# Kernel tuning notes

Hardware: AMD Instinct MI355X
Metric: run time of the kernel (lower is better)

## Reference

```python
import jax, jax.numpy as jnp
import numpy as np

N = 100000
D = 128
E = 1600000
NUM_STEPS = 8
LAM0 = 1.0
LAM1 = 1.0
ALPHA = 1.0 / (1.0 + 0.0 + LAM0 + LAM1)  # args.alp == 0 path


def setup_inputs() -> dict:
    key = jax.random.key(0)
    ks = jax.random.split(key, 12)
    X = jax.random.normal(ks[0], (N, D), dtype=jnp.float32)
    # H init: normal(0, 1/in_features) + I  (notresidual=False branch)
    H1 = jax.random.normal(ks[1], (D, D), dtype=jnp.float32) * (1.0 / D) + jnp.eye(D, dtype=jnp.float32)
    H2 = jax.random.normal(ks[2], (D, D), dtype=jnp.float32) * (1.0 / D) + jnp.eye(D, dtype=jnp.float32)
    w_beta = jax.random.uniform(ks[3], (E,), dtype=jnp.float32)
    w_gamma = jax.random.uniform(ks[4], (E,), dtype=jnp.float32)
    d_beta = jax.random.uniform(ks[5], (N,), dtype=jnp.float32)
    d_gamma = jax.random.uniform(ks[6], (N,), dtype=jnp.float32)
    src_beta = jax.random.randint(ks[7], (E,), 0, N, dtype=jnp.int32)
    dst_beta = jax.random.randint(ks[8], (E,), 0, N, dtype=jnp.int32)
    src_gamma = jax.random.randint(ks[9], (E,), 0, N, dtype=jnp.int32)
    dst_gamma = jax.random.randint(ks[10], (E,), 0, N, dtype=jnp.int32)
    return {"X": X, "H1": H1, "H2": H2, "w_beta": w_beta, "w_gamma": w_gamma,
            "d_beta": d_beta, "d_gamma": d_gamma,
            "src_beta": src_beta, "dst_beta": dst_beta,
            "src_gamma": src_gamma, "dst_gamma": dst_gamma}


def _spmm(w, src, dst, Y):
    # (sparse A) @ Y with A[dst, src] = w
    return jax.ops.segment_sum(w[:, None] * Y[src], dst, num_segments=N)


def reference(X, H1, H2, w_beta, w_gamma, d_beta, d_gamma,
              src_beta, dst_beta, src_gamma, dst_gamma):
    # Q_tild = lam0*D_beta + lam1*D_gamma + I  (diagonal)
    q = LAM0 * d_beta + LAM1 * d_gamma + 1.0  # [N]
    S1 = H1 + H1.T
    P1 = H1 @ H1.T
    S2 = H2 + H2.T
    P2 = H2 @ H2.T
    Y0 = X
    Y = X
    for _ in range(NUM_STEPS):
        AbY = _spmm(w_beta, src_beta, dst_beta, Y)    # A_beta @ Y
        AgY = _spmm(w_gamma, src_gamma, dst_gamma, Y)  # A_gamma @ Y
        term_beta = AbY @ S1 - d_beta[:, None] * (Y @ P1)
        # L_gamma @ Y = D_gamma@Y - A_gamma@Y
        term_gamma = (d_gamma[:, None] * Y - AgY
                      + AgY @ S2 - d_gamma[:, None] * (Y @ P2))
        Y_hat = LAM0 * term_beta + Y0 + LAM1 * term_gamma
        Y = (1.0 - ALPHA) * Y + ALPHA * (Y_hat / q[:, None])
    return Y
```

## Files before the change

kernel.cpp:

```cpp
#include <hip/hip_runtime.h>
#include <cstdint>
#include <cstddef>

#define DD 128


__global__ void count2_k(const int* __restrict__ dstb, const int* __restrict__ dstg,
                         int* __restrict__ degb, int* __restrict__ degg, int E, int gE) {
    int b = blockIdx.x;
    const int* dst = (b < gE) ? dstb : dstg;
    int* deg = (b < gE) ? degb : degg;
    int i = ((b < gE) ? b : b - gE) * blockDim.x + threadIdx.x;
    if (i < E) atomicAdd(&deg[dst[i]], 1);
}

__global__ __launch_bounds__(1024) void scan2_k(const int* __restrict__ degb,
                                                const int* __restrict__ degg,
                                                int* __restrict__ rpb, int* __restrict__ rpg,
                                                int* __restrict__ curb, int* __restrict__ curg,
                                                int n) {
    const int* deg = (blockIdx.x == 0) ? degb : degg;
    int* rp = (blockIdx.x == 0) ? rpb : rpg;
    int* cur = (blockIdx.x == 0) ? curb : curg;
    __shared__ int sums[1024];
    int tid = threadIdx.x;
    int per = (n + 1023) >> 10;
    int start = tid * per;
    int end = min(start + per, n);
    int s = 0;
    for (int i = start; i < end; ++i) s += deg[i];
    sums[tid] = s;
    __syncthreads();
    for (int off = 1; off < 1024; off <<= 1) {
        int v = (tid >= off) ? sums[tid - off] : 0;
        __syncthreads();
        sums[tid] += v;
        __syncthreads();
    }
    int pre = (tid == 0) ? 0 : sums[tid - 1];
    for (int i = start; i < end; ++i) {
        rp[i] = pre;
        cur[i] = pre;
        pre += deg[i];
    }
    if (end == n) rp[n] = pre;
}

__global__ void fill2_k(const int* __restrict__ srcb, const int* __restrict__ dstb,
                        const float* __restrict__ wb,
                        const int* __restrict__ srcg, const int* __restrict__ dstg,
                        const float* __restrict__ wg,
                        int* __restrict__ curb, int* __restrict__ curg,
                        int2* __restrict__ eb, int2* __restrict__ eg, int E, int gE) {
    int b = blockIdx.x;
    bool isb = (b < gE);
    const int* src = isb ? srcb : srcg;
    const int* dst = isb ? dstb : dstg;
    const float* w = isb ? wb : wg;
    int* cur = isb ? curb : curg;
    int2* edges = isb ? eb : eg;
    int i = (isb ? b : b - gE) * blockDim.x + threadIdx.x;
    if (i < E) {
        int d = dst[i];
        int pos = atomicAdd(&cur[d], 1);
        edges[pos] = make_int2(src[i], __float_as_int(w[i]));
    }
}


__global__ __launch_bounds__(256) void prep_k(const float* __restrict__ H,
                                              float* __restrict__ P,
                                              float* __restrict__ S) {
    int idx = blockIdx.x * 256 + threadIdx.x;
    int i = idx >> 7, j = idx & 127;
    float acc = 0.f;
    for (int k = 0; k < DD; ++k) acc += H[i * DD + k] * H[j * DD + k];
    P[idx] = acc;
    S[idx] = H[i * DD + j] + H[j * DD + i];
}


__global__ __launch_bounds__(256) void spmm_k(const int* __restrict__ rp,
                                              const int2* __restrict__ edges,
                                              const float* __restrict__ Y,
                                              float* __restrict__ out, int n) {
    int node = blockIdx.x * 4 + (threadIdx.x >> 6);
    if (node >= n) return;
    int lane = threadIdx.x & 63;
    int beg = rp[node], end = rp[node + 1];
    float a0 = 0.f, a1 = 0.f;
    int j = beg;
    for (; j + 8 <= end; j += 8) {
        int2 e0 = edges[j + 0], e1 = edges[j + 1], e2 = edges[j + 2], e3 = edges[j + 3];
        int2 e4 = edges[j + 4], e5 = edges[j + 5], e6 = edges[j + 6], e7 = edges[j + 7];
        float2 f0 = *((const float2*)(Y + (size_t)e0.x * DD) + lane);
        float2 f1 = *((const float2*)(Y + (size_t)e1.x * DD) + lane);
        float2 f2 = *((const float2*)(Y + (size_t)e2.x * DD) + lane);
        float2 f3 = *((const float2*)(Y + (size_t)e3.x * DD) + lane);
        float2 f4 = *((const float2*)(Y + (size_t)e4.x * DD) + lane);
        float2 f5 = *((const float2*)(Y + (size_t)e5.x * DD) + lane);
        float2 f6 = *((const float2*)(Y + (size_t)e6.x * DD) + lane);
        float2 f7 = *((const float2*)(Y + (size_t)e7.x * DD) + lane);
        float w0 = __int_as_float(e0.y), w1 = __int_as_float(e1.y);
        float w2 = __int_as_float(e2.y), w3 = __int_as_float(e3.y);
        float w4 = __int_as_float(e4.y), w5 = __int_as_float(e5.y);
        float w6 = __int_as_float(e6.y), w7 = __int_as_float(e7.y);
        a0 += w0 * f0.x; a1 += w0 * f0.y;
        a0 += w1 * f1.x; a1 += w1 * f1.y;
        a0 += w2 * f2.x; a1 += w2 * f2.y;
        a0 += w3 * f3.x; a1 += w3 * f3.y;
        a0 += w4 * f4.x; a1 += w4 * f4.y;
        a0 += w5 * f5.x; a1 += w5 * f5.y;
        a0 += w6 * f6.x; a1 += w6 * f6.y;
        a0 += w7 * f7.x; a1 += w7 * f7.y;
    }
    for (; j + 4 <= end; j += 4) {
        int2 e0 = edges[j + 0], e1 = edges[j + 1], e2 = edges[j + 2], e3 = edges[j + 3];
        float2 f0 = *((const float2*)(Y + (size_t)e0.x * DD) + lane);
        float2 f1 = *((const float2*)(Y + (size_t)e1.x * DD) + lane);
        float2 f2 = *((const float2*)(Y + (size_t)e2.x * DD) + lane);
        float2 f3 = *((const float2*)(Y + (size_t)e3.x * DD) + lane);
        float w0 = __int_as_float(e0.y), w1 = __int_as_float(e1.y);
        float w2 = __int_as_float(e2.y), w3 = __int_as_float(e3.y);
        a0 += w0 * f0.x; a1 += w0 * f0.y;
        a0 += w1 * f1.x; a1 += w1 * f1.y;
        a0 += w2 * f2.x; a1 += w2 * f2.y;
        a0 += w3 * f3.x; a1 += w3 * f3.y;
    }
    for (; j < end; ++j) {
        int2 e = edges[j];
        float2 f = *((const float2*)(Y + (size_t)e.x * DD) + lane);
        float wv = __int_as_float(e.y);
        a0 += wv * f.x; a1 += wv * f.y;
    }
    *((float2*)(out + (size_t)node * DD) + lane) = make_float2(a0, a1);
}


#define ATS 68
#define BS 160

__global__ __launch_bounds__(128, 2) void dense_k(
    const float* __restrict__ Y, const float* __restrict__ X,
    const float* __restrict__ Ab, const float* __restrict__ Ag,
    const float* __restrict__ db, const float* __restrict__ dg,
    const float* __restrict__ P1, const float* __restrict__ P2,
    const float* __restrict__ S1, const float* __restrict__ S2,
    float* __restrict__ Yn, int n)
{
    __shared__ float At[32 * ATS];
    __shared__ float B1[32 * BS];
    __shared__ float B2[32 * BS];

    const int tid = threadIdx.x;
    const int cg = tid & 15;
    const int rg = tid >> 4;
    const int row0 = blockIdx.x * 64;

    float aP1[8][8], aP2[8][8], aS[8][8];
#pragma unroll
    for (int i = 0; i < 8; ++i)
#pragma unroll
        for (int j = 0; j < 8; ++j) { aP1[i][j] = 0.f; aP2[i][j] = 0.f; aS[i][j] = 0.f; }

    auto stageA = [&](const float* __restrict__ G, int kq) {
        int r = tid >> 1;
        int kh = (tid & 1) * 16;
        int rowc = min(row0 + r, n - 1);
        const float* gp = G + (size_t)rowc * DD + kq * 32 + kh;
#pragma unroll
        for (int u = 0; u < 4; ++u) {
            float4 v = *reinterpret_cast<const float4*>(gp + 4 * u);
            int kb = kh + 4 * u;
            At[(kb + 0) * ATS + r] = v.x;
            At[(kb + 1) * ATS + r] = v.y;
            At[(kb + 2) * ATS + r] = v.z;
            At[(kb + 3) * ATS + r] = v.w;
        }
    };
    auto stageB = [&](const float* __restrict__ M, float* __restrict__ Bd, int kq) {
        int kl = tid >> 2;
        int cb = (tid & 3) * 32;
        const float* gp = M + (size_t)(kq * 32 + kl) * DD + cb;
        float* bp = Bd + kl * BS;
#pragma unroll
        for (int u = 0; u < 8; ++u) {
            float4 v = *reinterpret_cast<const float4*>(gp + 4 * u);
            int c = cb + 4 * u;
            float vv[4] = {v.x, v.y, v.z, v.w};
#pragma unroll
            for (int q = 0; q < 4; ++q) {
                int cc = c + q;
                bp[10 * (cc >> 3) + (cc & 7)] = vv[q];
            }
        }
    };

    const int abase = rg * 8;
    const int bbase = 10 * cg;

    for (int kq = 0; kq < 4; ++kq) {
        if (kq) __syncthreads();
        stageA(Y, kq);
        stageB(P1, B1, kq);
        stageB(P2, B2, kq);
        __syncthreads();
#pragma unroll 2
        for (int kl = 0; kl < 32; ++kl) {
            float a[8], b1[8], b2[8];
            *reinterpret_cast<float4*>(&a[0]) = *reinterpret_cast<const float4*>(&At[kl * ATS + abase]);
            *reinterpret_cast<float4*>(&a[4]) = *reinterpret_cast<const float4*>(&At[kl * ATS + abase + 4]);
#pragma unroll
            for (int m = 0; m < 4; ++m) {
                *reinterpret_cast<float2*>(&b1[2 * m]) = *reinterpret_cast<const float2*>(&B1[kl * BS + bbase + 2 * m]);
                *reinterpret_cast<float2*>(&b2[2 * m]) = *reinterpret_cast<const float2*>(&B2[kl * BS + bbase + 2 * m]);
            }
#pragma unroll
            for (int i = 0; i < 8; ++i)
#pragma unroll
                for (int j = 0; j < 8; ++j) {
                    aP1[i][j] += a[i] * b1[j];
                    aP2[i][j] += a[i] * b2[j];
                }
        }
    }
    __syncthreads();

    for (int kq = 0; kq < 4; ++kq) {
        if (kq) __syncthreads();
        stageA(Ab, kq);
        stageB(S1, B1, kq);
        __syncthreads();
#pragma unroll 2
        for (int kl = 0; kl < 32; ++kl) {
            float a[8], b1[8];
            *reinterpret_cast<float4*>(&a[0]) = *reinterpret_cast<const float4*>(&At[kl * ATS + abase]);
            *reinterpret_cast<float4*>(&a[4]) = *reinterpret_cast<const float4*>(&At[kl * ATS + abase + 4]);
#pragma unroll
            for (int m = 0; m < 4; ++m)
                *reinterpret_cast<float2*>(&b1[2 * m]) = *reinterpret_cast<const float2*>(&B1[kl * BS + bbase + 2 * m]);
#pragma unroll
            for (int i = 0; i < 8; ++i)
#pragma unroll
                for (int j = 0; j < 8; ++j) aS[i][j] += a[i] * b1[j];
        }
    }
    __syncthreads();

    for (int kq = 0; kq < 4; ++kq) {
        if (kq) __syncthreads();
        stageA(Ag, kq);
        stageB(S2, B1, kq);
        __syncthreads();
#pragma unroll 2
        for (int kl = 0; kl < 32; ++kl) {
            float a[8], b1[8];
            *reinterpret_cast<float4*>(&a[0]) = *reinterpret_cast<const float4*>(&At[kl * ATS + abase]);
            *reinterpret_cast<float4*>(&a[4]) = *reinterpret_cast<const float4*>(&At[kl * ATS + abase + 4]);
#pragma unroll
            for (int m = 0; m < 4; ++m)
                *reinterpret_cast<float2*>(&b1[2 * m]) = *reinterpret_cast<const float2*>(&B1[kl * BS + bbase + 2 * m]);
#pragma unroll
            for (int i = 0; i < 8; ++i)
#pragma unroll
                for (int j = 0; j < 8; ++j) aS[i][j] += a[i] * b1[j];
        }
    }

    const float AL = 1.0f / 3.0f;
#pragma unroll
    for (int i = 0; i < 8; ++i) {
        int row = row0 + rg * 8 + i;
        if (row < n) {
            float dbv = db[row], dgv = dg[row];
            float aq = AL / (dbv + dgv + 1.0f);
            size_t off = (size_t)row * DD + cg * 8;
            float4 y0 = *reinterpret_cast<const float4*>(Y + off);
            float4 y1 = *reinterpret_cast<const float4*>(Y + off + 4);
            float4 x0 = *reinterpret_cast<const float4*>(X + off);
            float4 x1 = *reinterpret_cast<const float4*>(X + off + 4);
            float4 g0 = *reinterpret_cast<const float4*>(Ag + off);
            float4 g1 = *reinterpret_cast<const float4*>(Ag + off + 4);
            float yv[8] = {y0.x, y0.y, y0.z, y0.w, y1.x, y1.y, y1.z, y1.w};
            float xv[8] = {x0.x, x0.y, x0.z, x0.w, x1.x, x1.y, x1.z, x1.w};
            float gv[8] = {g0.x, g0.y, g0.z, g0.w, g1.x, g1.y, g1.z, g1.w};
            float ov[8];
#pragma unroll
            for (int j = 0; j < 8; ++j) {
                float yhat = aS[i][j] - dbv * aP1[i][j] - dgv * aP2[i][j]
                             + xv[j] + dgv * yv[j] - gv[j];
                ov[j] = (1.0f - AL) * yv[j] + yhat * aq;
            }
            *reinterpret_cast<float4*>(Yn + off) = make_float4(ov[0], ov[1], ov[2], ov[3]);
            *reinterpret_cast<float4*>(Yn + off + 4) = make_float4(ov[4], ov[5], ov[6], ov[7]);
        }
    }
}


extern "C" void kernel_launch(void* const* d_in, const int* in_sizes, int n_in,
                              void* d_out, int out_size, void* d_ws, size_t ws_size,
                              hipStream_t stream) {
    const float* X   = (const float*)d_in[0];
    const float* H1  = (const float*)d_in[1];
    const float* H2  = (const float*)d_in[2];
    const float* wb  = (const float*)d_in[3];
    const float* wg  = (const float*)d_in[4];
    const float* db  = (const float*)d_in[5];
    const float* dg  = (const float*)d_in[6];
    const int* srcb  = (const int*)d_in[7];
    const int* dstb  = (const int*)d_in[8];
    const int* srcg  = (const int*)d_in[9];
    const int* dstg  = (const int*)d_in[10];
    const int N = in_sizes[5];
    const int E = in_sizes[3];
    float* Yout = (float*)d_out;

    char* p = (char*)d_ws;
    auto alloc = [&](size_t b) -> void* {
        void* r = (void*)p;
        p += (b + 255) & ~(size_t)255;
        return r;
    };
    float* P1 = (float*)alloc((size_t)DD * DD * 4);
    float* S1 = (float*)alloc((size_t)DD * DD * 4);
    float* P2 = (float*)alloc((size_t)DD * DD * 4);
    float* S2 = (float*)alloc((size_t)DD * DD * 4);
    int* degb = (int*)alloc((size_t)N * 4);
    int* degg = (int*)alloc((size_t)N * 4);
    int* rpb  = (int*)alloc((size_t)(N + 1) * 4);
    int* rpg  = (int*)alloc((size_t)(N + 1) * 4);
    int* curb = (int*)alloc((size_t)N * 4);
    int* curg = (int*)alloc((size_t)N * 4);
    int2* eb  = (int2*)alloc((size_t)E * 8);
    int2* eg  = (int2*)alloc((size_t)E * 8);
    float* AbY = (float*)alloc((size_t)N * DD * 4);
    float* AgY = (float*)alloc((size_t)N * DD * 4);
    float* Yw  = (float*)alloc((size_t)N * DD * 4);

    hipMemsetAsync(degb, 0, (size_t)N * 4, stream);
    hipMemsetAsync(degg, 0, (size_t)N * 4, stream);

    int gE = (E + 255) / 256;
    count2_k<<<2 * gE, 256, 0, stream>>>(dstb, dstg, degb, degg, E, gE);
    scan2_k<<<2, 1024, 0, stream>>>(degb, degg, rpb, rpg, curb, curg, N);
    fill2_k<<<2 * gE, 256, 0, stream>>>(srcb, dstb, wb, srcg, dstg, wg,
                                        curb, curg, eb, eg, E, gE);
    prep_k<<<64, 256, 0, stream>>>(H1, P1, S1);
    prep_k<<<64, 256, 0, stream>>>(H2, P2, S2);

    const float* Ycur = X;
    float* Ybufs[2] = {Yw, Yout};
    int gs = (N + 3) / 4;
    int gd = (N + 63) / 64;
    for (int s = 0; s < 8; ++s) {
        spmm_k<<<gs, 256, 0, stream>>>(rpb, eb, Ycur, AbY, N);
        spmm_k<<<gs, 256, 0, stream>>>(rpg, eg, Ycur, AgY, N);
        float* Yn = Ybufs[s & 1];
        dense_k<<<gd, 128, 0, stream>>>(Ycur, X, AbY, AgY, db, dg,
                                        P1, P2, S1, S2, Yn, N);
        Ycur = Yn;
    }
}
```

Before: 4.297 ms.

## Fuse SpMM gathers into dense step kernel, keeping aggregated tiles in shared memory

Merges the two SpMM kernels and the dense update into one per-step kernel. Each 256-thread block gathers A_beta@Y and A_gamma@Y rows for its 64-node tile straight into shared memory and multiplies by S1/S2 there, and the -A_gamma@Y term is read from shared memory. This removes the N x 128 AbY/AgY intermediates and their global write and read, plus two launches per step. The tradeoff is that the gather is serialized inside the block with syncs between phases. Occupancy now depends on the 256-thread block and its larger shared footprint (about 48 KB) instead of separate gather kernels with many small blocks, so load-latency hiding during the gather may be weaker.

```diff
diff --git a/kernel.cpp b/kernel.cpp
--- a/kernel.cpp
+++ b/kernel.cpp
@@ -3,6 +3,9 @@
 #include <cstddef>
 
 #define DD 128
+#define ATS 68
+#define ARS 132
+#define BQS 132
 
 
 __global__ void count2_k(const int* __restrict__ dstb, const int* __restrict__ dstg,
@@ -80,219 +83,173 @@
 }
 
 
-__global__ __launch_bounds__(256) void spmm_k(const int* __restrict__ rp,
-                                              const int2* __restrict__ edges,
-                                              const float* __restrict__ Y,
-                                              float* __restrict__ out, int n) {
-    int node = blockIdx.x * 4 + (threadIdx.x >> 6);
-    if (node >= n) return;
-    int lane = threadIdx.x & 63;
-    int beg = rp[node], end = rp[node + 1];
-    float a0 = 0.f, a1 = 0.f;
-    int j = beg;
-    for (; j + 8 <= end; j += 8) {
-        int2 e0 = edges[j + 0], e1 = edges[j + 1], e2 = edges[j + 2], e3 = edges[j + 3];
-        int2 e4 = edges[j + 4], e5 = edges[j + 5], e6 = edges[j + 6], e7 = edges[j + 7];
-        float2 f0 = *((const float2*)(Y + (size_t)e0.x * DD) + lane);
-        float2 f1 = *((const float2*)(Y + (size_t)e1.x * DD) + lane);
-        float2 f2 = *((const float2*)(Y + (size_t)e2.x * DD) + lane);
-        float2 f3 = *((const float2*)(Y + (size_t)e3.x * DD) + lane);
-        float2 f4 = *((const float2*)(Y + (size_t)e4.x * DD) + lane);
-        float2 f5 = *((const float2*)(Y + (size_t)e5.x * DD) + lane);
-        float2 f6 = *((const float2*)(Y + (size_t)e6.x * DD) + lane);
-        float2 f7 = *((const float2*)(Y + (size_t)e7.x * DD) + lane);
-        float w0 = __int_as_float(e0.y), w1 = __int_as_float(e1.y);
-        float w2 = __int_as_float(e2.y), w3 = __int_as_float(e3.y);
-        float w4 = __int_as_float(e4.y), w5 = __int_as_float(e5.y);
-        float w6 = __int_as_float(e6.y), w7 = __int_as_float(e7.y);
-        a0 += w0 * f0.x; a1 += w0 * f0.y;
-        a0 += w1 * f1.x; a1 += w1 * f1.y;
-        a0 += w2 * f2.x; a1 += w2 * f2.y;
-        a0 += w3 * f3.x; a1 += w3 * f3.y;
-        a0 += w4 * f4.x; a1 += w4 * f4.y;
-        a0 += w5 * f5.x; a1 += w5 * f5.y;
-        a0 += w6 * f6.x; a1 += w6 * f6.y;
-        a0 += w7 * f7.x; a1 += w7 * f7.y;
-    }
-    for (; j + 4 <= end; j += 4) {
-        int2 e0 = edges[j + 0], e1 = edges[j + 1], e2 = edges[j + 2], e3 = edges[j + 3];
-        float2 f0 = *((const float2*)(Y + (size_t)e0.x * DD) + lane);
-        float2 f1 = *((const float2*)(Y + (size_t)e1.x * DD) + lane);
-        float2 f2 = *((const float2*)(Y + (size_t)e2.x * DD) + lane);
-        float2 f3 = *((const float2*)(Y + (size_t)e3.x * DD) + lane);
-        float w0 = __int_as_float(e0.y), w1 = __int_as_float(e1.y);
-        float w2 = __int_as_float(e2.y), w3 = __int_as_float(e3.y);
-        a0 += w0 * f0.x; a1 += w0 * f0.y;
-        a0 += w1 * f1.x; a1 += w1 * f1.y;
-        a0 += w2 * f2.x; a1 += w2 * f2.y;
-        a0 += w3 * f3.x; a1 += w3 * f3.y;
-    }
-    for (; j < end; ++j) {
-        int2 e = edges[j];
-        float2 f = *((const float2*)(Y + (size_t)e.x * DD) + lane);
-        float wv = __int_as_float(e.y);
-        a0 += wv * f.x; a1 += wv * f.y;
-    }
-    *((float2*)(out + (size_t)node * DD) + lane) = make_float2(a0, a1);
-}
-
-
-#define ATS 68
-#define BS 160
-
-__global__ __launch_bounds__(128, 2) void dense_k(
-    const float* __restrict__ Y, const float* __restrict__ X,
-    const float* __restrict__ Ab, const float* __restrict__ Ag,
+__global__ __launch_bounds__(256, 3) void step_k(
+    const float* __restrict__ Yc, const float* __restrict__ X,
+    const int* __restrict__ rpb, const int2* __restrict__ eb,
+    const int* __restrict__ rpg, const int2* __restrict__ eg,
     const float* __restrict__ db, const float* __restrict__ dg,
     const float* __restrict__ P1, const float* __restrict__ P2,
     const float* __restrict__ S1, const float* __restrict__ S2,
     float* __restrict__ Yn, int n)
 {
-    __shared__ float At[32 * ATS];
-    __shared__ float B1[32 * BS];
-    __shared__ float B2[32 * BS];
+    __shared__ float At[DD * ATS];
+    __shared__ float U[32 * ARS];
 
     const int tid = threadIdx.x;
+    const int lane = tid & 63;
+    const int wv = tid >> 6;
     const int cg = tid & 15;
     const int rg = tid >> 4;
     const int row0 = blockIdx.x * 64;
 
-    float aP1[8][8], aP2[8][8], aS[8][8];
-#pragma unroll
-    for (int i = 0; i < 8; ++i)
-#pragma unroll
-        for (int j = 0; j < 8; ++j) { aP1[i][j] = 0.f; aP2[i][j] = 0.f; aS[i][j] = 0.f; }
-
-    auto stageA = [&](const float* __restrict__ G, int kq) {
-        int r = tid >> 1;
-        int kh = (tid & 1) * 16;
+    float aS[4][8], aP1[4][8], aP2[4][8];
+#pragma unroll
+    for (int i = 0; i < 4; ++i)
+#pragma unroll
+        for (int j = 0; j < 8; ++j) { aS[i][j] = 0.f; aP1[i][j] = 0.f; aP2[i][j] = 0.f; }
+
+    auto gatherA = [&](const int* __restrict__ rp, const int2* __restrict__ edges) {
+        for (int h = 0; h < 2; ++h) {
+#pragma unroll 1
+            for (int it = 0; it < 8; ++it) {
+                int r = wv * 8 + it;
+                int node = row0 + h * 32 + r;
+                float a0 = 0.f, a1 = 0.f;
+                if (node < n) {
+                    int beg = rp[node], end = rp[node + 1];
+                    int j = beg;
+                    for (; j + 4 <= end; j += 4) {
+                        int2 e0 = edges[j + 0], e1 = edges[j + 1];
+                        int2 e2 = edges[j + 2], e3 = edges[j + 3];
+                        float2 f0 = *((const float2*)(Yc + (size_t)e0.x * DD) + lane);
+                        float2 f1 = *((const float2*)(Yc + (size_t)e1.x * DD) + lane);
+                        float2 f2 = *((const float2*)(Yc + (size_t)e2.x * DD) + lane);
+                        float2 f3 = *((const float2*)(Yc + (size_t)e3.x * DD) + lane);
+                        float w0 = __int_as_float(e0.y), w1 = __int_as_float(e1.y);
+                        float w2 = __int_as_float(e2.y), w3 = __int_as_float(e3.y);
+                        a0 += w0 * f0.x; a1 += w0 * f0.y;
+                        a0 += w1 * f1.x; a1 += w1 * f1.y;
+                        a0 += w2 * f2.x; a1 += w2 * f2.y;
+                        a0 += w3 * f3.x; a1 += w3 * f3.y;
+                    }
+                    for (; j < end; ++j) {
+                        int2 e = edges[j];
+                        float2 f = *((const float2*)(Yc + (size_t)e.x * DD) + lane);
+                        float wv2 = __int_as_float(e.y);
+                        a0 += wv2 * f.x; a1 += wv2 * f.y;
+                    }
+                }
+                *reinterpret_cast<float2*>(&U[r * ARS + 2 * lane]) = make_float2(a0, a1);
+            }
+            __syncthreads();
+            {
+                int r = tid & 31;
+                int cb = (tid >> 5) * 16;
+#pragma unroll
+                for (int u = 0; u < 4; ++u) {
+                    float4 v = *reinterpret_cast<const float4*>(&U[r * ARS + cb + 4 * u]);
+                    int c = cb + 4 * u;
+                    At[(c + 0) * ATS + h * 32 + r] = v.x;
+                    At[(c + 1) * ATS + h * 32 + r] = v.y;
+                    At[(c + 2) * ATS + h * 32 + r] = v.z;
+                    At[(c + 3) * ATS + h * 32 + r] = v.w;
+                }
+            }
+            __syncthreads();
+        }
+    };
+
+    auto stageY = [&]() {
+        int r = tid >> 2;
         int rowc = min(row0 + r, n - 1);
-        const float* gp = G + (size_t)rowc * DD + kq * 32 + kh;
-#pragma unroll
-        for (int u = 0; u < 4; ++u) {
-            float4 v = *reinterpret_cast<const float4*>(gp + 4 * u);
-            int kb = kh + 4 * u;
-            At[(kb + 0) * ATS + r] = v.x;
-            At[(kb + 1) * ATS + r] = v.y;
-            At[(kb + 2) * ATS + r] = v.z;
-            At[(kb + 3) * ATS + r] = v.w;
+        const float* gp = Yc + (size_t)rowc * DD;
+#pragma unroll
+        for (int i = 0; i < 8; ++i) {
+            int c = ((tid & 3) << 2) + (i << 4);
+            float4 v = *reinterpret_cast<const float4*>(gp + c);
+            At[(c + 0) * ATS + r] = v.x;
+            At[(c + 1) * ATS + r] = v.y;
+            At[(c + 2) * ATS + r] = v.z;
+            At[(c + 3) * ATS + r] = v.w;
         }
     };
-    auto stageB = [&](const float* __restrict__ M, float* __restrict__ Bd, int kq) {
-        int kl = tid >> 2;
-        int cb = (tid & 3) * 32;
-        const float* gp = M + (size_t)(kq * 32 + kl) * DD + cb;
-        float* bp = Bd + kl * BS;
-#pragma unroll
-        for (int u = 0; u < 8; ++u) {
-            float4 v = *reinterpret_cast<const float4*>(gp + 4 * u);
-            int c = cb + 4 * u;
-            float vv[4] = {v.x, v.y, v.z, v.w};
-#pragma unroll
-            for (int q = 0; q < 4; ++q) {
-                int cc = c + q;
-                bp[10 * (cc >> 3) + (cc & 7)] = vv[q];
-            }
+
+    auto gemm = [&](const float* __restrict__ M, float (&acc)[4][8]) {
+#pragma unroll 1
+        for (int kq = 0; kq < 4; ++kq) {
+            {
+                int kl = tid & 31;
+                int cb = (tid >> 5) * 16;
+                const float* gp = M + (size_t)(kq * 32 + kl) * DD + cb;
+                float* bp = U + kl * BQS + cb;
+#pragma unroll
+                for (int u = 0; u < 4; ++u)
+                    *reinterpret_cast<float4*>(bp + 4 * u) =
+                        *reinterpret_cast<const float4*>(gp + 4 * u);
+            }
+            __syncthreads();
+#pragma unroll 2
+            for (int kl = 0; kl < 32; ++kl) {
+                int k = kq * 32 + kl;
+                float4 a = *reinterpret_cast<const float4*>(&At[k * ATS + rg * 4]);
+                float4 b0 = *reinterpret_cast<const float4*>(&U[kl * BQS + cg * 4]);
+                float4 b1 = *reinterpret_cast<const float4*>(&U[kl * BQS + 64 + cg * 4]);
+                float av[4] = {a.x, a.y, a.z, a.w};
+                float bv[8] = {b0.x, b0.y, b0.z, b0.w, b1.x, b1.y, b1.z, b1.w};
+#pragma unroll
+                for (int i = 0; i < 4; ++i)
+#pragma unroll
+                    for (int j = 0; j < 8; ++j) acc[i][j] += av[i] * bv[j];
+            }
+            __syncthreads();
         }
     };
 
-    const int abase = rg * 8;
-    const int bbase = 10 * cg;
-
-    for (int kq = 0; kq < 4; ++kq) {
-        if (kq) __syncthreads();
-        stageA(Y, kq);
-        stageB(P1, B1, kq);
-        stageB(P2, B2, kq);
-        __syncthreads();
-#pragma unroll 2
-        for (int kl = 0; kl < 32; ++kl) {
-            float a[8], b1[8], b2[8];
-            *reinterpret_cast<float4*>(&a[0]) = *reinterpret_cast<const float4*>(&At[kl * ATS + abase]);
-            *reinterpret_cast<float4*>(&a[4]) = *reinterpret_cast<const float4*>(&At[kl * ATS + abase + 4]);
-#pragma unroll
-            for (int m = 0; m < 4; ++m) {
-                *reinterpret_cast<float2*>(&b1[2 * m]) = *reinterpret_cast<const float2*>(&B1[kl * BS + bbase + 2 * m]);
-                *reinterpret_cast<float2*>(&b2[2 * m]) = *reinterpret_cast<const float2*>(&B2[kl * BS + bbase + 2 * m]);
-            }
-#pragma unroll
-            for (int i = 0; i < 8; ++i)
-#pragma unroll
-                for (int j = 0; j < 8; ++j) {
-                    aP1[i][j] += a[i] * b1[j];
-                    aP2[i][j] += a[i] * b2[j];
-                }
+    gatherA(rpb, eb);
+    gemm(S1, aS);
+
+    gatherA(rpg, eg);
+    gemm(S2, aS);
+#pragma unroll
+    for (int i = 0; i < 4; ++i) {
+        int r = rg * 4 + i;
+#pragma unroll
+        for (int j = 0; j < 8; ++j) {
+            int c = (j >> 2) * 64 + cg * 4 + (j & 3);
+            aS[i][j] -= At[c * ATS + r];
         }
     }
     __syncthreads();
 
-    for (int kq = 0; kq < 4; ++kq) {
-        if (kq) __syncthreads();
-        stageA(Ab, kq);
-        stageB(S1, B1, kq);
-        __syncthreads();
-#pragma unroll 2
-        for (int kl = 0; kl < 32; ++kl) {
-            float a[8], b1[8];
-            *reinterpret_cast<float4*>(&a[0]) = *reinterpret_cast<const float4*>(&At[kl * ATS + abase]);
-            *reinterpret_cast<float4*>(&a[4]) = *reinterpret_cast<const float4*>(&At[kl * ATS + abase + 4]);
-#pragma unroll
-            for (int m = 0; m < 4; ++m)
-                *reinterpret_cast<float2*>(&b1[2 * m]) = *reinterpret_cast<const float2*>(&B1[kl * BS + bbase + 2 * m]);
-#pragma unroll
-            for (int i = 0; i < 8; ++i)
-#pragma unroll
-                for (int j = 0; j < 8; ++j) aS[i][j] += a[i] * b1[j];
-        }
-    }
+    stageY();
     __syncthreads();
-
-    for (int kq = 0; kq < 4; ++kq) {
-        if (kq) __syncthreads();
-        stageA(Ag, kq);
-        stageB(S2, B1, kq);
-        __syncthreads();
-#pragma unroll 2
-        for (int kl = 0; kl < 32; ++kl) {
-            float a[8], b1[8];
-            *reinterpret_cast<float4*>(&a[0]) = *reinterpret_cast<const float4*>(&At[kl * ATS + abase]);
-            *reinterpret_cast<float4*>(&a[4]) = *reinterpret_cast<const float4*>(&At[kl * ATS + abase + 4]);
-#pragma unroll
-            for (int m = 0; m < 4; ++m)
-                *reinterpret_cast<float2*>(&b1[2 * m]) = *reinterpret_cast<const float2*>(&B1[kl * BS + bbase + 2 * m]);
-#pragma unroll
-            for (int i = 0; i < 8; ++i)
-#pragma unroll
-                for (int j = 0; j < 8; ++j) aS[i][j] += a[i] * b1[j];
-        }
-    }
+    gemm(P1, aP1);
+    gemm(P2, aP2);
 
     const float AL = 1.0f / 3.0f;
 #pragma unroll
-    for (int i = 0; i < 8; ++i) {
-        int row = row0 + rg * 8 + i;
+    for (int i = 0; i < 4; ++i) {
+        int row = row0 + rg * 4 + i;
         if (row < n) {
             float dbv = db[row], dgv = dg[row];
             float aq = AL / (dbv + dgv + 1.0f);
-            size_t off = (size_t)row * DD + cg * 8;
-            float4 y0 = *reinterpret_cast<const float4*>(Y + off);
-            float4 y1 = *reinterpret_cast<const float4*>(Y + off + 4);
-            float4 x0 = *reinterpret_cast<const float4*>(X + off);
-            float4 x1 = *reinterpret_cast<const float4*>(X + off + 4);
-            float4 g0 = *reinterpret_cast<const float4*>(Ag + off);
-            float4 g1 = *reinterpret_cast<const float4*>(Ag + off + 4);
-            float yv[8] = {y0.x, y0.y, y0.z, y0.w, y1.x, y1.y, y1.z, y1.w};
-            float xv[8] = {x0.x, x0.y, x0.z, x0.w, x1.x, x1.y, x1.z, x1.w};
-            float gv[8] = {g0.x, g0.y, g0.z, g0.w, g1.x, g1.y, g1.z, g1.w};
-            float ov[8];
-#pragma unroll
-            for (int j = 0; j < 8; ++j) {
-                float yhat = aS[i][j] - dbv * aP1[i][j] - dgv * aP2[i][j]
-                             + xv[j] + dgv * yv[j] - gv[j];
-                ov[j] = (1.0f - AL) * yv[j] + yhat * aq;
-            }
-            *reinterpret_cast<float4*>(Yn + off) = make_float4(ov[0], ov[1], ov[2], ov[3]);
-            *reinterpret_cast<float4*>(Yn + off + 4) = make_float4(ov[4], ov[5], ov[6], ov[7]);
+#pragma unroll
+            for (int hh = 0; hh < 2; ++hh) {
+                size_t off = (size_t)row * DD + hh * 64 + cg * 4;
+                float4 y = *reinterpret_cast<const float4*>(Yc + off);
+                float4 x = *reinterpret_cast<const float4*>(X + off);
+                float yv[4] = {y.x, y.y, y.z, y.w};
+                float xv[4] = {x.x, x.y, x.z, x.w};
+                float ov[4];
+#pragma unroll
+                for (int q = 0; q < 4; ++q) {
+                    int j = hh * 4 + q;
+                    float yhat = aS[i][j] - dbv * aP1[i][j] - dgv * aP2[i][j]
+                                 + xv[q] + dgv * yv[q];
+                    ov[q] = (1.0f - AL) * yv[q] + yhat * aq;
+                }
+                *reinterpret_cast<float4*>(Yn + off) = make_float4(ov[0], ov[1], ov[2], ov[3]);
+            }
         }
     }
 }
@@ -334,8 +291,6 @@
     int* curg = (int*)alloc((size_t)N * 4);
     int2* eb  = (int2*)alloc((size_t)E * 8);
     int2* eg  = (int2*)alloc((size_t)E * 8);
-    float* AbY = (float*)alloc((size_t)N * DD * 4);
-    float* AgY = (float*)alloc((size_t)N * DD * 4);
     float* Yw  = (float*)alloc((size_t)N * DD * 4);
 
     hipMemsetAsync(degb, 0, (size_t)N * 4, stream);
@@ -351,14 +306,11 @@
 
     const float* Ycur = X;
     float* Ybufs[2] = {Yw, Yout};
-    int gs = (N + 3) / 4;
     int gd = (N + 63) / 64;
     for (int s = 0; s < 8; ++s) {
-        spmm_k<<<gs, 256, 0, stream>>>(rpb, eb, Ycur, AbY, N);
-        spmm_k<<<gs, 256, 0, stream>>>(rpg, eg, Ycur, AgY, N);
         float* Yn = Ybufs[s & 1];
-        dense_k<<<gd, 128, 0, stream>>>(Ycur, X, AbY, AgY, db, dg,
-                                        P1, P2, S1, S2, Yn, N);
+        step_k<<<gd, 256, 0, stream>>>(Ycur, X, rpb, eb, rpg, eg, db, dg,
+                                       P1, P2, S1, S2, Yn, N);
         Ycur = Yn;
     }
 }
```

New measurement: 4.771 ms. +11.0%, slower.
